# Optimization experiments

Hardware: AMD Instinct MI355X
Metric: run time of the kernel (lower is better)

## Reference

```python
import jax, jax.numpy as jnp
import numpy as np

MASK_SUB = 1000000.0  # the module subtracts 1e6 from masked scores (not -inf)

def setup_inputs() -> dict:
    key = jax.random.key(0)
    kq, kk, kv = jax.random.split(key, 3)
    B, S, D = 16, 2048, 64
    q = jax.random.normal(kq, (B, S, D), dtype=jnp.float32)
    k = jax.random.normal(kk, (B, S, D), dtype=jnp.float32)
    v = jax.random.normal(kv, (B, S, D), dtype=jnp.float32)
    return {"q": q, "k": k, "v": v}

def reference(q, k, v):
    d_k = k.shape[-1]
    s = k.shape[-2]
    # scores: [b, s_q, s_k]
    scores = jnp.einsum('bqd,bkd->bqk', q, k) / jnp.sqrt(jnp.asarray(d_k, q.dtype))
    # causal mask: strictly-upper-triangular entries get 1e6 subtracted (matches torch.triu diagonal=1)
    causal = jnp.triu(jnp.ones((s, s), dtype=bool), k=1)
    scores = jnp.where(causal[None, :, :], scores - MASK_SUB, scores)
    weights = jax.nn.softmax(scores, axis=-1)
    return jnp.einsum('bqk,bkd->bqd', weights, v)
```

## Files before the change

### kernel.cpp

```cpp
#include <hip/hip_runtime.h>
#include <stdint.h>


typedef __bf16 bf16x8 __attribute__((ext_vector_type(8)));
typedef float f32x4 __attribute__((ext_vector_type(4)));
typedef float f32x16 __attribute__((ext_vector_type(16)));
typedef uint32_t u32x4 __attribute__((ext_vector_type(4)));

#define NB 16
#define SL 2048
#define DH 64

__device__ __forceinline__ __bf16 f2bf(float f) {
    uint32_t u = __builtin_bit_cast(uint32_t, f);
    u += 0x7FFFu + ((u >> 16) & 1u);
    uint16_t h = (uint16_t)(u >> 16);
    return __builtin_bit_cast(__bf16, h);
}

__device__ __forceinline__ uint32_t cvtpk(float lo, float hi) {
    uint32_t r;
    asm("v_cvt_pk_bf16_f32 %0, %1, %2" : "=v"(r) : "v"(lo), "v"(hi));
    return r;
}

__device__ __forceinline__ void load_lds16(const void* g, void* l) {
    __builtin_amdgcn_global_load_lds(
        (const __attribute__((address_space(1))) uint32_t*)g,
        (__attribute__((address_space(3))) uint32_t*)l, 16, 0, 0);
}

__global__ __launch_bounds__(256) void prepass(
        const float* __restrict__ K, const float* __restrict__ V,
        __bf16* __restrict__ Kb, __bf16* __restrict__ Vt) {
    __shared__ float tl[64][68];
    const int b    = blockIdx.x >> 5;
    const int tile = blockIdx.x & 31;
    const int s0   = tile << 6;
    const int t    = threadIdx.x;
    const int r    = t >> 2;
    const int c0   = (t & 3) * 16;

    const float* Kp = K + ((size_t)(b * SL + s0) + r) * DH + c0;
    float4 f0 = ((const float4*)Kp)[0], f1 = ((const float4*)Kp)[1];
    float4 f2 = ((const float4*)Kp)[2], f3 = ((const float4*)Kp)[3];
    bf16x8 w0, w1;
    w0[0]=f2bf(f0.x); w0[1]=f2bf(f0.y); w0[2]=f2bf(f0.z); w0[3]=f2bf(f0.w);
    w0[4]=f2bf(f1.x); w0[5]=f2bf(f1.y); w0[6]=f2bf(f1.z); w0[7]=f2bf(f1.w);
    w1[0]=f2bf(f2.x); w1[1]=f2bf(f2.y); w1[2]=f2bf(f2.z); w1[3]=f2bf(f2.w);
    w1[4]=f2bf(f3.x); w1[5]=f2bf(f3.y); w1[6]=f2bf(f3.z); w1[7]=f2bf(f3.w);
    __bf16* Kbp = Kb + ((size_t)(b * SL + s0) + r) * DH;
    const int j0 = c0 >> 3;
    *(bf16x8*)(Kbp + ((j0       ^ (r & 7)) * 8)) = w0;
    *(bf16x8*)(Kbp + (((j0 + 1) ^ (r & 7)) * 8)) = w1;

    const float* Vp = V + ((size_t)(b * SL + s0) + r) * DH + c0;
    ((float4*)&tl[r][c0])[0] = ((const float4*)Vp)[0];
    ((float4*)&tl[r][c0])[1] = ((const float4*)Vp)[1];
    ((float4*)&tl[r][c0])[2] = ((const float4*)Vp)[2];
    ((float4*)&tl[r][c0])[3] = ((const float4*)Vp)[3];
    __syncthreads();

    __bf16* img = Vt + ((size_t)(b * 32 + tile)) * 4096;
#pragma unroll
    for (int half = 0; half < 2; ++half) {
        const int c = half * 256 + t;
        const int d = c >> 3, slot = c & 7;
        const int jj = slot ^ (d & 7);
        bf16x8 w;
#pragma unroll
        for (int e = 0; e < 8; ++e) w[e] = f2bf(tl[jj * 8 + e][d]);
        *(bf16x8*)(img + c * 8) = w;
    }
}

__global__ __launch_bounds__(256, 3) void attn_fwd(
        const float* __restrict__ Q, const __bf16* __restrict__ Kb,
        const __bf16* __restrict__ Vt, float* __restrict__ part,
        float* __restrict__ lpart) {
    __shared__ __align__(16) __bf16 lK[3][4096];
    __shared__ __align__(16) __bf16 lV[3][4096];

    const int bid = blockIdx.x;
    const int b   = bid & 15;
    const int j   = 39 - (bid >> 4);
    int qb, c;
    if (j < 4)        { qb = j;                 c = 0; }
    else if (j < 12)  { qb = 4 + ((j - 4) >> 1);  c = (j - 4) & 1; }
    else if (j < 24)  { int k = j - 12; qb = 8 + k / 3;    c = k % 3; }
    else              { int k = j - 24; qb = 12 + (k >> 2); c = k & 3; }
    const int nt  = 2 * qb + 2;
    const int kt0 = c * 8;
    const int kt1 = min(kt0 + 8, nt);

    const int tid  = threadIdx.x;
    const int wave = tid >> 6, lane = tid & 63;
    const int h    = lane >> 5, l32 = lane & 31, x8 = lane & 7;
    const int qg   = qb * 128 + wave * 32 + l32;
    const int dt   = 2 * qb + (wave >> 1);

    const float QSC = 0.125f * 1.44269504088896340736f;
    bf16x8 qf[4];
    const float* qp = Q + ((size_t)b * SL + qg) * DH + h * 8;
#pragma unroll
    for (int s4 = 0; s4 < 4; ++s4) {
        float4 a0 = ((const float4*)(qp + s4 * 16))[0];
        float4 a1 = ((const float4*)(qp + s4 * 16))[1];
        qf[s4][0] = f2bf(a0.x * QSC); qf[s4][1] = f2bf(a0.y * QSC);
        qf[s4][2] = f2bf(a0.z * QSC); qf[s4][3] = f2bf(a0.w * QSC);
        qf[s4][4] = f2bf(a1.x * QSC); qf[s4][5] = f2bf(a1.y * QSC);
        qf[s4][6] = f2bf(a1.z * QSC); qf[s4][7] = f2bf(a1.w * QSC);
    }

    f32x16 acc0 = (f32x16)0.0f, acc1 = (f32x16)0.0f;
    float lsa0 = 0.f, lsa1 = 0.f, lsa2 = 0.f, lsa3 = 0.f;

    const __bf16* Kbase = Kb + (size_t)b * SL * DH;
    const __bf16* Vbase = Vt + (size_t)b * 32 * 4096;

    auto stage = [&](int ti, int bufi) {
        const __bf16* Ks = Kbase + (size_t)ti * 4096;
        const __bf16* Vs = Vbase + (size_t)ti * 4096;
#pragma unroll
        for (int i2 = 0; i2 < 2; ++i2) {
            load_lds16(Ks + (size_t)(i2 * 256 + tid) * 8,
                       &lK[bufi][(i2 * 256 + wave * 64) * 8]);
            load_lds16(Vs + (size_t)(i2 * 256 + tid) * 8,
                       &lV[bufi][(i2 * 256 + wave * 64) * 8]);
        }
    };

    __builtin_amdgcn_sched_barrier(0);
    stage(kt0, kt0 % 3);
    stage(min(kt0 + 1, 31), (kt0 + 1) % 3);
    stage(min(kt0 + 2, 31), (kt0 + 2) % 3);

    for (int kt = kt0; kt < kt1; ++kt) {
        asm volatile("s_waitcnt vmcnt(8)" ::: "memory");
        asm volatile("s_barrier" ::: "memory");
        const __bf16* K_ = lK[kt % 3];
        const __bf16* V_ = lV[kt % 3];

        const bool skip = (wave < 2) && (kt == nt - 1);
        if (!skip) {
            f32x16 sc0 = (f32x16)0.0f, sc1 = (f32x16)0.0f;
            __builtin_amdgcn_s_setprio(1);
#pragma unroll
            for (int s4 = 0; s4 < 4; ++s4) {
                bf16x8 kf0 = *(const bf16x8*)&K_[(l32)      * 64 + (((s4 * 2 + h) ^ x8) << 3)];
                bf16x8 kf1 = *(const bf16x8*)&K_[(32 + l32) * 64 + (((s4 * 2 + h) ^ x8) << 3)];
                sc0 = __builtin_amdgcn_mfma_f32_32x32x16_bf16(kf0, qf[s4], sc0, 0, 0, 0);
                sc1 = __builtin_amdgcn_mfma_f32_32x32x16_bf16(kf1, qf[s4], sc1, 0, 0, 0);
            }
            __builtin_amdgcn_s_setprio(0);

            if (kt >= dt) {
                const int kb = kt * 64;
#pragma unroll
                for (int r = 0; r < 16; ++r) {
                    const int krow = (r & 3) + 8 * (r >> 2) + 4 * h;
                    if (kb + krow > qg)      sc0[r] = -1.0e30f;
                    if (kb + 32 + krow > qg) sc1[r] = -1.0e30f;
                }
            }

#pragma unroll
            for (int r = 0; r < 16; ++r) {
                sc0[r] = __builtin_amdgcn_exp2f(sc0[r]);
                sc1[r] = __builtin_amdgcn_exp2f(sc1[r]);
            }
#pragma unroll
            for (int r = 0; r < 16; r += 4) {
                lsa0 += sc0[r + 0] + sc1[r + 0];
                lsa1 += sc0[r + 1] + sc1[r + 1];
                lsa2 += sc0[r + 2] + sc1[r + 2];
                lsa3 += sc0[r + 3] + sc1[r + 3];
            }

            bf16x8 af[4];
#pragma unroll
            for (int ks = 0; ks < 4; ++ks) {
                const int jj = (ks & 1) * 8;
                const f32x16& sg = (ks & 2) ? sc1 : sc0;
                uint32_t u0 = cvtpk(sg[jj + 0], sg[jj + 1]);
                uint32_t u1 = cvtpk(sg[jj + 2], sg[jj + 3]);
                uint32_t u2 = cvtpk(sg[jj + 4], sg[jj + 5]);
                uint32_t u3 = cvtpk(sg[jj + 6], sg[jj + 7]);
                auto r0 = __builtin_amdgcn_permlane32_swap(u0, u2, false, false);
                auto r1 = __builtin_amdgcn_permlane32_swap(u1, u3, false, false);
                u32x4 w; w[0] = r0[0]; w[1] = r1[0]; w[2] = r0[1]; w[3] = r1[1];
                af[ks] = __builtin_bit_cast(bf16x8, w);
            }

            __builtin_amdgcn_s_setprio(1);
#pragma unroll
            for (int ks = 0; ks < 4; ++ks) {
                bf16x8 vf0 = *(const bf16x8*)&V_[(l32)      * 64 + ((((ks << 1) + h) ^ x8) << 3)];
                bf16x8 vf1 = *(const bf16x8*)&V_[(32 + l32) * 64 + ((((ks << 1) + h) ^ x8) << 3)];
                acc0 = __builtin_amdgcn_mfma_f32_32x32x16_bf16(af[ks], vf0, acc0, 0, 0, 0);
                acc1 = __builtin_amdgcn_mfma_f32_32x32x16_bf16(af[ks], vf1, acc1, 0, 0, 0);
            }
            __builtin_amdgcn_s_setprio(0);
        }

        asm volatile("s_barrier" ::: "memory");
        stage(min(kt + 3, 31), kt % 3);
    }

    asm volatile("s_waitcnt vmcnt(0)" ::: "memory");

    float ls = (lsa0 + lsa1) + (lsa2 + lsa3);
    ls += __shfl_xor(ls, 32);

#pragma unroll
    for (int r = 0; r < 16; ++r) {
        const int qrow = qb * 128 + wave * 32 + (r & 3) + 8 * (r >> 2) + 4 * h;
        float* pp = part + ((size_t)(b * SL + qrow) * 4 + c) * DH + l32;
        pp[0]  = acc0[r];
        pp[32] = acc1[r];
    }
    if (h == 0)
        lpart[(size_t)(b * SL + qg) * 4 + c] = ls;
}

__global__ __launch_bounds__(256) void combine(
        const float* __restrict__ part, const float* __restrict__ lpart,
        float* __restrict__ O) {
    const int tid = threadIdx.x;
    const int r   = blockIdx.x * 16 + (tid >> 4);
    const int d4  = tid & 15;
    const int qb  = (r >> 7) & 15;
    const int nch = (2 * qb + 9) >> 3;
    float4 s = make_float4(0.f, 0.f, 0.f, 0.f);
    float ls = 0.f;
    for (int c = 0; c < nch; ++c) {
        float4 p = *(const float4*)(part + ((size_t)r * 4 + c) * DH + d4 * 4);
        s.x += p.x; s.y += p.y; s.z += p.z; s.w += p.w;
        ls += lpart[(size_t)r * 4 + c];
    }
    const float inv = 1.0f / ls;
    float4 o; o.x = s.x * inv; o.y = s.y * inv; o.z = s.z * inv; o.w = s.w * inv;
    *(float4*)(O + (size_t)r * DH + d4 * 4) = o;
}

extern "C" void kernel_launch(void* const* d_in, const int* in_sizes, int n_in,
                              void* d_out, int out_size, void* d_ws, size_t ws_size,
                              hipStream_t stream) {
    const float* q = (const float*)d_in[0];
    const float* k = (const float*)d_in[1];
    const float* v = (const float*)d_in[2];
    float* o = (float*)d_out;
    __bf16* Kb   = (__bf16*)d_ws;
    __bf16* Vt   = Kb + (size_t)NB * SL * DH;
    float*  pt   = (float*)((char*)d_ws + (8u << 20));
    float*  lp   = pt + (size_t)NB * SL * 4 * DH;
    hipLaunchKernelGGL(prepass, dim3(NB * 32), dim3(256), 0, stream, k, v, Kb, Vt);
    hipLaunchKernelGGL(attn_fwd, dim3(640), dim3(256), 0, stream, q, Kb, Vt, pt, lp);
    hipLaunchKernelGGL(combine, dim3(NB * SL / 16), dim3(256), 0, stream, pt, lp, o);
}
```

Before: 96.78 us.

## Write single-chunk query blocks directly and store split partials as bf16

Query blocks whose causal range fits in a single key chunk (the first 512 rows) now normalise their output inside the attention kernel and write it straight to O. They skip the partial buffer and the combine pass, and the combine grid shrinks to cover only rows 512 and above. Partial accumulators for the remaining rows are stored as bf16 instead of fp32, which halves partial-buffer traffic at the cost of extra rounding error in the unnormalised sums. A block-wide barrier and a small shared array are added so each wave can read the row sums it needs.

```diff
diff --git a/kernel.cpp b/kernel.cpp
--- a/kernel.cpp
+++ b/kernel.cpp
@@ -16,6 +16,10 @@
     u += 0x7FFFu + ((u >> 16) & 1u);
     uint16_t h = (uint16_t)(u >> 16);
     return __builtin_bit_cast(__bf16, h);
+}
+
+__device__ __forceinline__ float bf2f(uint16_t u) {
+    return __builtin_bit_cast(float, (uint32_t)u << 16);
 }
 
 __device__ __forceinline__ uint32_t cvtpk(float lo, float hi) {
@@ -76,10 +80,11 @@
 
 __global__ __launch_bounds__(256, 3) void attn_fwd(
         const float* __restrict__ Q, const __bf16* __restrict__ Kb,
-        const __bf16* __restrict__ Vt, float* __restrict__ part,
-        float* __restrict__ lpart) {
+        const __bf16* __restrict__ Vt, __bf16* __restrict__ part,
+        float* __restrict__ lpart, float* __restrict__ O) {
     __shared__ __align__(16) __bf16 lK[3][4096];
     __shared__ __align__(16) __bf16 lV[3][4096];
+    __shared__ float lsw[128];
 
     const int bid = blockIdx.x;
     const int b   = bid & 15;
@@ -90,6 +95,7 @@
     else if (j < 24)  { int k = j - 12; qb = 8 + k / 3;    c = k % 3; }
     else              { int k = j - 24; qb = 12 + (k >> 2); c = k & 3; }
     const int nt  = 2 * qb + 2;
+    const int nch = (2 * qb + 9) >> 3;
     const int kt0 = c * 8;
     const int kt1 = min(kt0 + 8, nt);
 
@@ -211,36 +217,54 @@
 
     float ls = (lsa0 + lsa1) + (lsa2 + lsa3);
     ls += __shfl_xor(ls, 32);
+    if (h == 0) lsw[wave * 32 + l32] = ls;
+    __syncthreads();
+
+    if (nch == 1) {
+        float* Ob = O + ((size_t)(b * SL + qb * 128 + wave * 32)) * DH;
+#pragma unroll
+        for (int r = 0; r < 16; ++r) {
+            const int crow = (r & 3) + 8 * (r >> 2) + 4 * h;
+            const float inv = 1.0f / lsw[wave * 32 + crow];
+            Ob[(size_t)crow * DH + l32]      = acc0[r] * inv;
+            Ob[(size_t)crow * DH + l32 + 32] = acc1[r] * inv;
+        }
+        return;
+    }
 
 #pragma unroll
     for (int r = 0; r < 16; ++r) {
         const int qrow = qb * 128 + wave * 32 + (r & 3) + 8 * (r >> 2) + 4 * h;
-        float* pp = part + ((size_t)(b * SL + qrow) * 4 + c) * DH + l32;
-        pp[0]  = acc0[r];
-        pp[32] = acc1[r];
+        __bf16* pp = part + ((size_t)(b * SL + qrow) * 4 + c) * DH + l32;
+        pp[0]  = f2bf(acc0[r]);
+        pp[32] = f2bf(acc1[r]);
     }
     if (h == 0)
         lpart[(size_t)(b * SL + qg) * 4 + c] = ls;
 }
 
 __global__ __launch_bounds__(256) void combine(
-        const float* __restrict__ part, const float* __restrict__ lpart,
+        const __bf16* __restrict__ part, const float* __restrict__ lpart,
         float* __restrict__ O) {
     const int tid = threadIdx.x;
-    const int r   = blockIdx.x * 16 + (tid >> 4);
+    const int bpb = 96;
+    const int b   = blockIdx.x / bpb;
+    const int ri  = blockIdx.x % bpb;
+    const int lrow = 512 + ri * 16 + (tid >> 4);
+    const size_t r = (size_t)b * SL + lrow;
     const int d4  = tid & 15;
-    const int qb  = (r >> 7) & 15;
+    const int qb  = lrow >> 7;
     const int nch = (2 * qb + 9) >> 3;
     float4 s = make_float4(0.f, 0.f, 0.f, 0.f);
     float ls = 0.f;
     for (int c = 0; c < nch; ++c) {
-        float4 p = *(const float4*)(part + ((size_t)r * 4 + c) * DH + d4 * 4);
-        s.x += p.x; s.y += p.y; s.z += p.z; s.w += p.w;
-        ls += lpart[(size_t)r * 4 + c];
+        ushort4 u = *(const ushort4*)(part + (r * 4 + c) * DH + d4 * 4);
+        s.x += bf2f(u.x); s.y += bf2f(u.y); s.z += bf2f(u.z); s.w += bf2f(u.w);
+        ls += lpart[r * 4 + c];
     }
     const float inv = 1.0f / ls;
     float4 o; o.x = s.x * inv; o.y = s.y * inv; o.z = s.z * inv; o.w = s.w * inv;
-    *(float4*)(O + (size_t)r * DH + d4 * 4) = o;
+    *(float4*)(O + r * DH + d4 * 4) = o;
 }
 
 extern "C" void kernel_launch(void* const* d_in, const int* in_sizes, int n_in,
@@ -252,9 +276,9 @@
     float* o = (float*)d_out;
     __bf16* Kb   = (__bf16*)d_ws;
     __bf16* Vt   = Kb + (size_t)NB * SL * DH;
-    float*  pt   = (float*)((char*)d_ws + (8u << 20));
-    float*  lp   = pt + (size_t)NB * SL * 4 * DH;
+    __bf16* pt   = (__bf16*)((char*)d_ws + (8u << 20));
+    float*  lp   = (float*)((char*)d_ws + (24u << 20));
     hipLaunchKernelGGL(prepass, dim3(NB * 32), dim3(256), 0, stream, k, v, Kb, Vt);
-    hipLaunchKernelGGL(attn_fwd, dim3(640), dim3(256), 0, stream, q, Kb, Vt, pt, lp);
-    hipLaunchKernelGGL(combine, dim3(NB * SL / 16), dim3(256), 0, stream, pt, lp, o);
-}
+    hipLaunchKernelGGL(attn_fwd, dim3(640), dim3(256), 0, stream, q, Kb, Vt, pt, lp, o);
+    hipLaunchKernelGGL(combine, dim3(NB * 96), dim3(256), 0, stream, pt, lp, o);
+}
```

New measurement: 96.43 us (median of 2 runs). Within noise of the previous version (-0.4%).
